# Kernel tuning notes

Hardware: AMD Instinct MI355X
Metric: run time of the kernel (lower is better)

The kernel has to match this reference:

```python
import jax, jax.numpy as jnp
import numpy as np

S = 1            # support_num
NEIGHBOR = 32    # neighbor_num for ball query
EPS = 1e-12

def _gather(t, idx):
    # t: (bs, N, C), idx: (bs, M, n) -> (bs, M, n, C)
    return jax.vmap(lambda tb, ib: tb[ib])(t, idx)

def _pick(t, idx):
    # t: (bs, M, C), idx: (bs, V) -> (bs, V, C)
    return jax.vmap(lambda tb, ib: tb[ib])(t, idx)

def _normalize(x, axis):
    return x / jnp.maximum(jnp.linalg.norm(x, axis=axis, keepdims=True), EPS)

def query_ball_point(radius, nsample, xyz, new_xyz):
    # PointNet++-style ball query: indices of first nsample points within radius,
    # missing slots filled with the first valid neighbor (self, since dist=0).
    sq = jnp.sum((new_xyz[:, :, None, :] - xyz[:, None, :, :]) ** 2, axis=-1)  # (bs,S,N)
    N = xyz.shape[1]
    idx = jnp.broadcast_to(jnp.arange(N), sq.shape)
    idx = jnp.where(sq > radius * radius, N, idx)
    idx = jnp.sort(idx, axis=-1)[:, :, :nsample]
    return jnp.where(idx == N, idx[:, :, :1], idx)

def _dir_norm(vertices, nbr_idx):
    nbrs = _gather(vertices, nbr_idx)                       # (bs,v,n,3)
    return _normalize(nbrs - vertices[:, :, None, :], axis=-1)

def conv_surface(nbr_idx, vertices, directions, K=32):
    # directions: (3, S*K)
    dn = _dir_norm(vertices, nbr_idx)
    theta = jax.nn.relu(jnp.einsum('bvnd,dk->bvnk', dn, _normalize(directions, 0)))
    bs, v, n, _ = theta.shape
    return theta.reshape(bs, v, n, S, K).max(axis=2).sum(axis=2)  # (bs,v,K)

def conv_layer(nbr_idx, vertices, fm, w, b, d, K=32):
    # w: (Cin,(S+1)*K), b: ((S+1)*K,), d: (3,S*K)
    dn = _dir_norm(vertices, nbr_idx)
    theta = jax.nn.relu(jnp.einsum('bvnd,dk->bvnk', dn, _normalize(d, 0)))  # (bs,v,n,S*K)
    f = jnp.einsum('bvc,ck->bvk', fm, w) + b                # (bs,v,(S+1)*K)
    center, support = f[..., :K], f[..., K:]
    sup = _gather(support, nbr_idx)                          # (bs,v,n,S*K)
    bs, v, n, _ = sup.shape
    act = (theta * sup).reshape(bs, v, n, S, K).max(axis=2).sum(axis=2)
    return center + act

def pool_layer(vertices, fm, radius, key, rate=4, nn_num=4):
    idx = query_ball_point(radius, nn_num, vertices, vertices)
    pooled = _gather(fm, idx).max(axis=2)                    # neighborhood max-pool
    v = vertices.shape[1]
    perm = jax.random.permutation(key, v)[: v // rate]       # random subsample (fixed key)
    return vertices[:, perm], pooled[:, perm]

def get_nearest_index(target, source):
    sq = jnp.sum((target[:, :, None, :] - source[:, None, :, :]) ** 2, axis=-1)
    return jnp.argmin(sq, axis=-1)                           # (bs, V_target)

def _forward(vertices, onehot, d0, w1, b1, dd1, w2, b2, dd2, w3, b3, dd3,
             w4, b4, dd4, w5, b5, dd5, w6, b6, dd6, w7, b7, dd7,
             cw1, cb1, cw2, cb2, cw3, cb3):
    relu = jax.nn.relu
    bs, V, _ = vertices.shape
    ni = query_ball_point(0.25, NEIGHBOR, vertices, vertices)
    fm0 = relu(conv_surface(ni, vertices, d0))
    fm1 = jnp.concatenate([fm0, relu(conv_layer(ni, vertices, fm0, w1, b1, dd1))], -1)
    fm2 = jnp.concatenate([fm1, relu(conv_layer(ni, vertices, fm1, w2, b2, dd2))], -1)
    v1, fp1 = pool_layer(vertices, fm2, 0.25, jax.random.fold_in(jax.random.key(42), 1))
    ni = query_ball_point(0.39, NEIGHBOR, v1, v1)
    fm3 = jnp.concatenate([fp1, relu(conv_layer(ni, v1, fp1, w3, b3, dd3))], -1)
    fm4 = jnp.concatenate([fm3, relu(conv_layer(ni, v1, fm3, w4, b4, dd4))], -1)
    fm5 = jnp.concatenate([fm4, relu(conv_layer(ni, v1, fm4, w5, b5, dd5))], -1)
    v2, fp2 = pool_layer(v1, fm5, 0.39, jax.random.fold_in(jax.random.key(42), 2))
    ni = query_ball_point(0.63, NEIGHBOR, v2, v2)
    fm6 = jnp.concatenate([fp2, relu(conv_layer(ni, v2, fp2, w6, b6, dd6))], -1)
    fm7 = jnp.concatenate([fm6, relu(conv_layer(ni, v2, fm6, w7, b7, dd7))], -1)
    f_global = fm7.max(axis=1)                               # (bs, 256)
    n1 = get_nearest_index(vertices, v1)
    n2 = get_nearest_index(vertices, v2)
    fuse = jnp.concatenate([
        fm0, fm1, fm2,
        _pick(fm3, n1), _pick(fm4, n1), _pick(fm5, n1),
        _pick(fm6, n2), _pick(fm7, n2),
        jnp.broadcast_to(f_global[:, None, :], (bs, V, f_global.shape[-1])),
        jnp.broadcast_to(onehot[:, None, :], (bs, V, onehot.shape[-1])),
    ], axis=-1)                                              # (bs, V, 1424)
    h = relu(jnp.einsum('bvc,oc->bvo', fuse, cw1) + cb1)
    h = relu(jnp.einsum('bvc,oc->bvo', h, cw2) + cb2)
    return jnp.einsum('bvc,oc->bvo', h, cw3) + cb3           # (bs, V, class_num)


def setup_inputs() -> dict:
    key = jax.random.key(0)
    ks = iter(jax.random.split(key, 40))
    bs, N, cat = 8, 2048, 16
    vertices = jax.random.uniform(next(ks), (bs, N, 3), dtype=jnp.float32)
    labels = jax.random.randint(next(ks), (bs,), 0, cat)
    onehot = jax.nn.one_hot(labels, cat, dtype=jnp.float32)
    def p(shape):
        return jax.random.normal(next(ks), shape, dtype=jnp.float32) * 0.05
    inp = {"vertices": vertices, "onehot": onehot, "d0": p((3, S * 32))}
    ins = [32, 64, 96, 128, 160, 192, 224]
    for i, c in enumerate(ins, start=1):
        inp[f"w{i}"] = p((c, (S + 1) * 32))
        inp[f"b{i}"] = p(((S + 1) * 32,))
        inp[f"dd{i}"] = p((3, S * 32))
    inp["cw1"] = p((1024, 1424)); inp["cb1"] = p((1024,))
    inp["cw2"] = p((512, 1024)); inp["cb2"] = p((512,))
    inp["cw3"] = p((50, 512)); inp["cb3"] = p((50,))
    return inp


def reference(vertices, onehot, d0, w1, b1, dd1, w2, b2, dd2, w3, b3, dd3,
              w4, b4, dd4, w5, b5, dd5, w6, b6, dd6, w7, b7, dd7,
              cw1, cb1, cw2, cb2, cw3, cb3):
    return _forward(vertices, onehot, d0, w1, b1, dd1, w2, b2, dd2, w3, b3, dd3,
                    w4, b4, dd4, w5, b5, dd5, w6, b6, dd6, w7, b7, dd7,
                    cw1, cb1, cw2, cb2, cw3, cb3)
```

## Files before the change

kernel.cpp:

```cpp
#include <hip/hip_runtime.h>
#include <hip/hip_bf16.h>

#define BS 8
#define V0 2048
#define V1N 512
#define V2N 128

typedef unsigned short ushort_t;
typedef __attribute__((ext_vector_type(8))) short bf16x8;
typedef __attribute__((ext_vector_type(4))) float f32x4;

__device__ __forceinline__ void tf2x32(unsigned k0, unsigned k1,
                                       unsigned x0, unsigned x1,
                                       unsigned &o0, unsigned &o1) {
  unsigned ks2 = k0 ^ k1 ^ 0x1BD11BDAu;
  x0 += k0; x1 += k1;
#define RR(r) { x0 += x1; x1 = (x1 << (r)) | (x1 >> (32 - (r))); x1 ^= x0; }
  RR(13) RR(15) RR(26) RR(6)   x0 += k1;  x1 += ks2 + 1u;
  RR(17) RR(29) RR(16) RR(24)  x0 += ks2; x1 += k0 + 2u;
  RR(13) RR(15) RR(26) RR(6)   x0 += k0;  x1 += k1 + 3u;
  RR(17) RR(29) RR(16) RR(24)  x0 += k1;  x1 += ks2 + 4u;
  RR(13) RR(15) RR(26) RR(6)   x0 += ks2; x1 += k0 + 5u;
#undef RR
  o0 = x0; o1 = x1;
}

__device__ __forceinline__ ushort_t f2bf(float f) {
  unsigned u = __float_as_uint(f);
  u += 0x7FFFu + ((u >> 16) & 1u);
  return (ushort_t)(u >> 16);
}

__device__ __forceinline__ float sqdist_f32(float cx, float cy, float cz,
                                            const float* p) {
  float dx = __fsub_rn(cx, p[0]);
  float dy = __fsub_rn(cy, p[1]);
  float dz = __fsub_rn(cz, p[2]);
  return __fadd_rn(__fadd_rn(__fmul_rn(dx, dx), __fmul_rn(dy, dy)),
                   __fmul_rn(dz, dz));
}

#define KP1 1472

#define PREP_BLKS 1025
#define QBP1_BLKS 512
__global__ __launch_bounds__(256) void misc1_kernel(
    int* __restrict__ rank, const float* __restrict__ cw1,
    const float* __restrict__ cw2, const float* __restrict__ cw3,
    const float* __restrict__ cb3, ushort_t* __restrict__ cw1b,
    ushort_t* __restrict__ cw2b, ushort_t* __restrict__ cw3b,
    float* __restrict__ cb3p, const float* __restrict__ pts,
    int* __restrict__ ni1) {
  int bid = blockIdx.x, tid = threadIdx.x;
  if (bid < 18) {
    __shared__ unsigned sb[2048];
    int seg, segfirst, n, base;
    if (bid < 8)       { seg = 0; segfirst = 0;  n = 2048; base = 0; }
    else if (bid < 16) { seg = 1; segfirst = 8;  n = 2048; base = 2048; }
    else               { seg = 2; segfirst = 16; n = 512;  base = 4096; }
    unsigned k0, k1, nk0, nk1, sk0, sk1;
    if (seg == 0) {
      tf2x32(0u, 42u, 0u, 1u, k0, k1);
      tf2x32(k0, k1, 0u, 1u, sk0, sk1);
    } else if (seg == 1) {
      tf2x32(0u, 42u, 0u, 1u, k0, k1);
      tf2x32(k0, k1, 0u, 0u, nk0, nk1);
      tf2x32(nk0, nk1, 0u, 1u, sk0, sk1);
    } else {
      tf2x32(0u, 42u, 0u, 2u, k0, k1);
      tf2x32(k0, k1, 0u, 1u, sk0, sk1);
    }
    for (int i = tid; i < n; i += 256) {
      unsigned o0, o1;
      tf2x32(sk0, sk1, 0u, (unsigned)i, o0, o1);
      sb[i] = o0 ^ o1;
    }
    __syncthreads();
    int tt = (bid - segfirst) * 256 + tid;
    unsigned bt = sb[tt];
    int cnt = 0;
#pragma unroll 8
    for (int s = 0; s < n; ++s) {
      unsigned bs = sb[s];
      cnt += (bs < bt) || (bs == bt && s < tt);
    }
    rank[base + tt] = cnt;
  } else if (bid < 18 + PREP_BLKS) {
    int c = (bid - 18) * 256 + tid;
    const int C1 = 1024 * (KP1 / 8);
    const int C2 = (512 * 1024) / 8;
    const int C3 = (128 * 512) / 8;
    if (c < C1) {
      int n = c / (KP1 / 8);
      int cc = c - n * (KP1 / 8);
      int k = cc * 8;
      bf16x8 o = (bf16x8){0, 0, 0, 0, 0, 0, 0, 0};
      if (k < 1424) {
        const float* src = cw1 + (size_t)n * 1424 + k;
        float4 lo = *(const float4*)src;
        float4 hi = *(const float4*)(src + 4);
        o[0] = (short)f2bf(lo.x); o[1] = (short)f2bf(lo.y);
        o[2] = (short)f2bf(lo.z); o[3] = (short)f2bf(lo.w);
        o[4] = (short)f2bf(hi.x); o[5] = (short)f2bf(hi.y);
        o[6] = (short)f2bf(hi.z); o[7] = (short)f2bf(hi.w);
      }
      *(bf16x8*)(cw1b + (size_t)c * 8) = o;
    } else if (c < C1 + C2) {
      int u = (c - C1) * 8;
      const float* src = cw2 + u;
      float4 lo = *(const float4*)src;
      float4 hi = *(const float4*)(src + 4);
      bf16x8 o;
      o[0] = (short)f2bf(lo.x); o[1] = (short)f2bf(lo.y);
      o[2] = (short)f2bf(lo.z); o[3] = (short)f2bf(lo.w);
      o[4] = (short)f2bf(hi.x); o[5] = (short)f2bf(hi.y);
      o[6] = (short)f2bf(hi.z); o[7] = (short)f2bf(hi.w);
      *(bf16x8*)(cw2b + u) = o;
    } else if (c < C1 + C2 + C3) {
      int u = (c - C1 - C2) * 8;
      int n = u >> 9, k = u & 511;
      bf16x8 o = (bf16x8){0, 0, 0, 0, 0, 0, 0, 0};
      if (n < 50) {
        const float* src = cw3 + (size_t)n * 512 + k;
        float4 lo = *(const float4*)src;
        float4 hi = *(const float4*)(src + 4);
        o[0] = (short)f2bf(lo.x); o[1] = (short)f2bf(lo.y);
        o[2] = (short)f2bf(lo.z); o[3] = (short)f2bf(lo.w);
        o[4] = (short)f2bf(hi.x); o[5] = (short)f2bf(hi.y);
        o[6] = (short)f2bf(hi.z); o[7] = (short)f2bf(hi.w);
      }
      *(bf16x8*)(cw3b + u) = o;
    } else if (c < C1 + C2 + C3 + 16) {
      int u = (c - C1 - C2 - C3) * 8;
#pragma unroll
      for (int e = 0; e < 8; ++e)
        cb3p[u + e] = (u + e) < 50 ? cb3[u + e] : 0.f;
    }
  } else {
    __shared__ float spts[V0 * 3];
    int bq = bid - 18 - PREP_BLKS;
    int qbase = bq * 32;
    int b = qbase >> 11;
    const float* base = pts + (size_t)b * V0 * 3;
    for (int i = tid; i < V0 * 3 / 4; i += 256)
      ((float4*)spts)[i] = ((const float4*)base)[i];
    __syncthreads();
    int lane = tid & 63, wv = tid >> 6;
    for (int rep = 0; rep < 8; ++rep) {
      int qoff = wv * 8 + rep;
      int qi = (qbase & 2047) + qoff;
      int wid = qbase + qoff;
      float cx = spts[qi * 3], cy = spts[qi * 3 + 1], cz = spts[qi * 3 + 2];
      int cnt = 0, idx0 = 0;
      for (int j0 = 0; j0 < V0; j0 += 64) {
        int j = j0 + lane;
        float d2 = sqdist_f32(cx, cy, cz, spts + (size_t)j * 3);
        bool in = (d2 <= 0.0625f);
        unsigned long long mask = __ballot(in);
        if (cnt == 0 && mask) idx0 = j0 + __builtin_ctzll(mask);
        if (in) {
          int rk = cnt + __popcll(mask & ((1ull << lane) - 1ull));
          if (rk < 32) ni1[(size_t)wid * 32 + rk] = j;
        }
        cnt += __popcll(mask);
        if (cnt >= 32) break;
      }
      for (int s = cnt + lane; s < 32; s += 64) ni1[(size_t)wid * 32 + s] = idx0;
    }
  }
}

__device__ __forceinline__ void dirn(const float* base, int v, int nb,
                                     float& ox, float& oy, float& oz) {
  float dx = __fsub_rn(base[nb * 3 + 0], base[v * 3 + 0]);
  float dy = __fsub_rn(base[nb * 3 + 1], base[v * 3 + 1]);
  float dz = __fsub_rn(base[nb * 3 + 2], base[v * 3 + 2]);
  float s2 = __fadd_rn(__fadd_rn(__fmul_rn(dx, dx), __fmul_rn(dy, dy)),
                       __fmul_rn(dz, dz));
  float nrm = fmaxf(__fsqrt_rn(s2), 1e-12f);
  ox = __fdiv_rn(dx, nrm); oy = __fdiv_rn(dy, nrm); oz = __fdiv_rn(dz, nrm);
}

__device__ __forceinline__ void norm_col(const float* d, int k,
                                         float& ox, float& oy, float& oz) {
  float x = d[k], y = d[32 + k], z = d[64 + k];
  float s2 = __fadd_rn(__fadd_rn(__fmul_rn(x, x), __fmul_rn(y, y)),
                       __fmul_rn(z, z));
  float nrm = fmaxf(__fsqrt_rn(s2), 1e-12f);
  ox = __fdiv_rn(x, nrm); oy = __fdiv_rn(y, nrm); oz = __fdiv_rn(z, nrm);
}

__global__ __launch_bounds__(256) void misc2_kernel(
    const int* __restrict__ rank, int* __restrict__ perm1,
    int* __restrict__ perm2, const float* __restrict__ pts,
    const int* __restrict__ ni, const float* __restrict__ d0,
    const float* __restrict__ w1, const float* __restrict__ b1,
    float* __restrict__ out, float* __restrict__ fn) {
  int bid = blockIdx.x, tid = threadIdx.x;
  if (bid == 0) {
    __shared__ int a1[2048];
    __shared__ int a2[2048];
    for (int i = tid; i < 2048; i += 256) a1[rank[i]] = i;
    __syncthreads();
    for (int i = tid; i < 2048; i += 256) a2[rank[2048 + i]] = a1[i];
    __syncthreads();
    for (int i = tid; i < 512; i += 256) perm1[i] = a2[i];
    for (int i = tid; i < 512; i += 256) a1[rank[4096 + i]] = i;
    __syncthreads();
    for (int i = tid; i < 128; i += 256) perm2[i] = a1[i];
    return;
  }
  __shared__ float sdir[3][32];
  __shared__ float sdn[8][32][3];
  __shared__ float sfm[8][32];
  if (tid < 32) {
    float x, y, z; norm_col(d0, tid, x, y, z);
    sdir[0][tid] = x; sdir[1][tid] = y; sdir[2][tid] = z;
  }
  int vloc = tid >> 5, k = tid & 31;
  size_t bvg = (size_t)(bid - 1) * 8 + vloc;
  int b = (int)(bvg >> 11), v = (int)(bvg & 2047);
  const float* base = pts + (size_t)b * V0 * 3;
  int nb = ni[bvg * 32 + k];
  float x, y, z; dirn(base, v, nb, x, y, z);
  sdn[vloc][k][0] = x; sdn[vloc][k][1] = y; sdn[vloc][k][2] = z;
  __syncthreads();
  float m = 0.f;
  for (int n = 0; n < 32; ++n) {
    float d = sdn[vloc][n][0] * sdir[0][k] + sdn[vloc][n][1] * sdir[1][k] +
              sdn[vloc][n][2] * sdir[2][k];
    m = fmaxf(m, fmaxf(d, 0.f));
  }
  out[bvg * 96 + k] = m;
  sfm[vloc][k] = m;
  __syncthreads();
  float a1v = b1[k], a2v = b1[k + 32];
  for (int c = 0; c < 32; ++c) {
    float vv = sfm[vloc][c];
    a1v += vv * w1[c * 64 + k];
    a2v += vv * w1[c * 64 + k + 32];
  }
  fn[bvg * 64 + k] = a1v;
  fn[bvg * 64 + k + 32] = a2v;
}

__global__ __launch_bounds__(256) void conv_act_kernel(
    const float* __restrict__ pts, const float* __restrict__ dd,
    const int* __restrict__ ni, const float* __restrict__ f,
    float* __restrict__ out, int Nv, int ldout, int colofs,
    const float* __restrict__ wn, const float* __restrict__ bn,
    float* __restrict__ fn) {
  __shared__ float sdir[3][32];
  __shared__ float sdn[8][32][3];
  __shared__ int sidx[8][32];
  __shared__ float sfm[8][256];
  int tid = threadIdx.x;
  if (tid < 32) {
    float x, y, z; norm_col(dd, tid, x, y, z);
    sdir[0][tid] = x; sdir[1][tid] = y; sdir[2][tid] = z;
  }
  int vloc = tid >> 5, k = tid & 31;
  size_t bvg = (size_t)blockIdx.x * 8 + vloc;
  int b = (int)(bvg / Nv), v = (int)(bvg % Nv);
  const float* base = pts + (size_t)b * Nv * 3;
  int nb = ni[bvg * 32 + k];
  float x, y, z; dirn(base, v, nb, x, y, z);
  sdn[vloc][k][0] = x; sdn[vloc][k][1] = y; sdn[vloc][k][2] = z;
  sidx[vloc][k] = nb;
  __syncthreads();
  float m = -INFINITY;
  size_t fb = (size_t)b * Nv * 64;
  for (int n = 0; n < 32; ++n) {
    float th = fmaxf(sdn[vloc][n][0] * sdir[0][k] + sdn[vloc][n][1] * sdir[1][k] +
                     sdn[vloc][n][2] * sdir[2][k], 0.f);
    float sup = f[fb + (size_t)sidx[vloc][n] * 64 + 32 + k];
    m = fmaxf(m, th * sup);
  }
  float center = f[bvg * 64 + k];
  float res = fmaxf(center + m, 0.f);
  out[bvg * ldout + colofs + k] = res;
  if (wn) {
    size_t rowbase = (size_t)blockIdx.x * 8;
#pragma unroll 1
    for (int r = 0; r < 8; ++r)
      if (tid < colofs) sfm[r][tid] = out[(rowbase + r) * ldout + tid];
    sfm[vloc][colofs + k] = res;
    __syncthreads();
    int cin = colofs + 32;
    float a1v = bn[k], a2v = bn[k + 32];
    for (int c = 0; c < cin; ++c) {
      float vv = sfm[vloc][c];
      a1v += vv * wn[c * 64 + k];
      a2v += vv * wn[c * 64 + k + 32];
    }
    fn[bvg * 64 + k] = a1v;
    fn[bvg * 64 + k + 32] = a2v;
  }
}

__global__ __launch_bounds__(256) void conv_act_qbp_kernel(
    const float* __restrict__ pts, int Nv, float rrq,
    const float* __restrict__ dd, int* __restrict__ ni_out,
    const float* __restrict__ f, float* __restrict__ out, int ldout,
    int colofs, const float* __restrict__ wn, const float* __restrict__ bn,
    float* __restrict__ fn) {
  __shared__ float spts[512 * 3];
  __shared__ float sdir[3][32];
  __shared__ float sdn[8][32][3];
  __shared__ int sni[8][32];
  __shared__ float sfm[8][256];
  int tid = threadIdx.x;
  int b = (blockIdx.x * 8) / Nv;
  int vbase = (blockIdx.x * 8) % Nv;
  const float* gp = pts + (size_t)b * Nv * 3;
  for (int i = tid; i < Nv * 3; i += 256) spts[i] = gp[i];
  if (tid < 32) {
    float x, y, z; norm_col(dd, tid, x, y, z);
    sdir[0][tid] = x; sdir[1][tid] = y; sdir[2][tid] = z;
  }
  __syncthreads();
  int lane = tid & 63, wv = tid >> 6;
  for (int rep = 0; rep < 2; ++rep) {
    int vl = wv * 2 + rep;
    int v = vbase + vl;
    float cx = spts[v * 3], cy = spts[v * 3 + 1], cz = spts[v * 3 + 2];
    int cnt = 0, idx0 = 0;
    for (int j0 = 0; j0 < Nv; j0 += 64) {
      int j = j0 + lane;
      float d2 = sqdist_f32(cx, cy, cz, spts + (size_t)j * 3);
      bool in = (d2 <= rrq);
      unsigned long long mask = __ballot(in);
      if (cnt == 0 && mask) idx0 = j0 + __builtin_ctzll(mask);
      if (in) {
        int rk = cnt + __popcll(mask & ((1ull << lane) - 1ull));
        if (rk < 32) sni[vl][rk] = j;
      }
      cnt += __popcll(mask);
      if (cnt >= 32) break;
    }
    for (int s = cnt + lane; s < 32; s += 64) sni[vl][s] = idx0;
  }
  __syncthreads();
  ni_out[(size_t)(blockIdx.x * 8) * 32 + tid] = sni[tid >> 5][tid & 31];
  int vloc = tid >> 5, k = tid & 31;
  size_t bvg = (size_t)blockIdx.x * 8 + vloc;
  int v = vbase + vloc;
  int nb = sni[vloc][k];
  float x, y, z; dirn(spts, v, nb, x, y, z);
  sdn[vloc][k][0] = x; sdn[vloc][k][1] = y; sdn[vloc][k][2] = z;
  __syncthreads();
  float m = -INFINITY;
  size_t fb = (size_t)b * Nv * 64;
  for (int n = 0; n < 32; ++n) {
    float th = fmaxf(sdn[vloc][n][0] * sdir[0][k] + sdn[vloc][n][1] * sdir[1][k] +
                     sdn[vloc][n][2] * sdir[2][k], 0.f);
    float sup = f[fb + (size_t)sni[vloc][n] * 64 + 32 + k];
    m = fmaxf(m, th * sup);
  }
  float center = f[bvg * 64 + k];
  float res = fmaxf(center + m, 0.f);
  out[bvg * ldout + colofs + k] = res;
  size_t rowbase = (size_t)blockIdx.x * 8;
#pragma unroll 1
  for (int r = 0; r < 8; ++r)
    if (tid < colofs) sfm[r][tid] = out[(rowbase + r) * ldout + tid];
  sfm[vloc][colofs + k] = res;
  __syncthreads();
  int cin = colofs + 32;
  float a1v = bn[k], a2v = bn[k + 32];
  for (int c = 0; c < cin; ++c) {
    float vv = sfm[vloc][c];
    a1v += vv * wn[c * 64 + k];
    a2v += vv * wn[c * 64 + k + 32];
  }
  fn[bvg * 64 + k] = a1v;
  fn[bvg * 64 + k + 32] = a2v;
}

__global__ __launch_bounds__(256) void pool_kernel(
    const float* __restrict__ pts_in, const float* __restrict__ fm_in,
    int ld_in, int C, int Nv_in, const int* __restrict__ perm, int Nv_out,
    float rr, float* __restrict__ pts_out, float* __restrict__ fm_out,
    int ld_out, const float* __restrict__ wn, const float* __restrict__ bn,
    float* __restrict__ fn) {
  __shared__ float spf[4][192];
  int wv = threadIdx.x >> 6;
  int lane = threadIdx.x & 63;
  int wid = blockIdx.x * 4 + wv;
  int b = wid / Nv_out, pp = wid - b * Nv_out;
  int v = perm[pp];
  const float* base = pts_in + (size_t)b * Nv_in * 3;
  float cx = base[v * 3], cy = base[v * 3 + 1], cz = base[v * 3 + 2];
  int nb[4]; int cnt = 0;
  for (int j0 = 0; j0 < Nv_in && cnt < 4; j0 += 64) {
    int j = j0 + lane;
    float d2 = sqdist_f32(cx, cy, cz, base + (size_t)j * 3);
    unsigned long long mask = __ballot(d2 <= rr);
    while (mask && cnt < 4) {
      int bp = __builtin_ctzll(mask);
      mask &= mask - 1;
      nb[cnt++] = j0 + bp;
    }
  }
  for (int q = cnt; q < 4; ++q) nb[q] = nb[0];
  if (lane < 3) pts_out[(size_t)wid * 3 + lane] = base[v * 3 + lane];
  size_t inrow = (size_t)b * Nv_in;
  size_t outrow = (size_t)wid * ld_out;
  for (int c = lane; c < C; c += 64) {
    float m = fm_in[(inrow + nb[0]) * ld_in + c];
    m = fmaxf(m, fm_in[(inrow + nb[1]) * ld_in + c]);
    m = fmaxf(m, fm_in[(inrow + nb[2]) * ld_in + c]);
    m = fmaxf(m, fm_in[(inrow + nb[3]) * ld_in + c]);
    fm_out[outrow + c] = m;
    spf[wv][c] = m;
  }
  __syncthreads();
  int o = threadIdx.x & 63, w_ = threadIdx.x >> 6;
  int wid0 = blockIdx.x * 4 + w_;
  float a = bn[o];
  for (int c = 0; c < C; ++c) a += spf[w_][c] * wn[c * 64 + o];
  fn[(size_t)wid0 * 64 + o] = a;
}

__global__ __launch_bounds__(256) void gmax_kernel(
    const float* __restrict__ fm, float* __restrict__ out) {
  __shared__ float red[8][32];
  int b = blockIdx.x >> 3, cg = blockIdx.x & 7;
  int vsub = threadIdx.x >> 5, cl = threadIdx.x & 31;
  int c = cg * 32 + cl;
  float m = -INFINITY;
  for (int v = vsub; v < V2N; v += 8)
    m = fmaxf(m, fm[((size_t)b * V2N + v) * 256 + c]);
  red[vsub][cl] = m;
  __syncthreads();
  if (vsub == 0) {
#pragma unroll
    for (int r = 1; r < 8; ++r) m = fmaxf(m, red[r][cl]);
    out[b * 256 + c] = m;
  }
}

__global__ __launch_bounds__(256) void fuse_row_kernel(
    const float* __restrict__ fm2, const float* __restrict__ fm5,
    const float* __restrict__ fm7, const float* __restrict__ fglob,
    const float* __restrict__ onehot, const float* __restrict__ verts,
    const float* __restrict__ v1, const float* __restrict__ v2,
    ushort_t* __restrict__ fuse_b) {
  __shared__ unsigned long long sred[8];
  __shared__ int sn12[2];
  int bv = blockIdx.x;
  int b = bv >> 11;
  int tid = threadIdx.x;
  int lane = tid & 63, wv = tid >> 6;
  float cx = verts[(size_t)bv * 3 + 0];
  float cy = verts[(size_t)bv * 3 + 1];
  float cz = verts[(size_t)bv * 3 + 2];
  unsigned long long b1 = ~0ull, b2 = ~0ull;
  const float* s1 = v1 + (size_t)b * V1N * 3;
  for (int j = tid; j < V1N; j += 256) {
    float d2 = sqdist_f32(cx, cy, cz, s1 + (size_t)j * 3);
    unsigned long long key =
        (((unsigned long long)__float_as_uint(d2)) << 32) | (unsigned)j;
    b1 = b1 < key ? b1 : key;
  }
  const float* s2 = v2 + (size_t)b * V2N * 3;
  if (tid < V2N) {
    float d2 = sqdist_f32(cx, cy, cz, s2 + (size_t)tid * 3);
    b2 = (((unsigned long long)__float_as_uint(d2)) << 32) | (unsigned)tid;
  }
#pragma unroll
  for (int off = 32; off > 0; off >>= 1) {
    unsigned long long o1 = __shfl_down(b1, off);
    unsigned long long o2 = __shfl_down(b2, off);
    b1 = b1 < o1 ? b1 : o1;
    b2 = b2 < o2 ? b2 : o2;
  }
  if (lane == 0) { sred[wv] = b1; sred[4 + wv] = b2; }
  __syncthreads();
  if (tid == 0) {
    unsigned long long m1 = sred[0], m2 = sred[4];
#pragma unroll
    for (int r = 1; r < 4; ++r) {
      m1 = m1 < sred[r] ? m1 : sred[r];
      m2 = m2 < sred[4 + r] ? m2 : sred[4 + r];
    }
    sn12[0] = (int)(m1 & 0xffffffffu);
    sn12[1] = (int)(m2 & 0xffffffffu);
  }
  __syncthreads();
  int sn1 = sn12[0], sn2 = sn12[1];
  const float* r2 = fm2 + (size_t)bv * 96;
  const float* r5 = fm5 + ((size_t)b * V1N + sn1) * 192;
  const float* r7 = fm7 + ((size_t)b * V2N + sn2) * 256;
  const float* rg = fglob + b * 256;
  const float* roh = onehot + b * 16;
  if (tid < KP1 / 8) {
    int c = tid * 8;
    const float* src = nullptr;
    if (c < 192) {
      int cc = (c < 32) ? c : (c < 96 ? c - 32 : c - 96);
      src = r2 + cc;
    } else if (c < 672) {
      int cc = (c < 320) ? c - 192 : (c < 480 ? c - 320 : c - 480);
      src = r5 + cc;
    } else if (c < 1152) {
      int cc = (c < 896) ? c - 672 : c - 896;
      src = r7 + cc;
    } else if (c < 1408) {
      src = rg + (c - 1152);
    } else if (c < 1424) {
      src = roh + (c - 1408);
    }
    float4 lo = make_float4(0.f, 0.f, 0.f, 0.f), hi = lo;
    if (src) { lo = *(const float4*)src; hi = *(const float4*)(src + 4); }
    bf16x8 o;
    o[0] = (short)f2bf(lo.x); o[1] = (short)f2bf(lo.y);
    o[2] = (short)f2bf(lo.z); o[3] = (short)f2bf(lo.w);
    o[4] = (short)f2bf(hi.x); o[5] = (short)f2bf(hi.y);
    o[6] = (short)f2bf(hi.z); o[7] = (short)f2bf(hi.w);
    *(bf16x8*)(fuse_b + (size_t)bv * KP1 + c) = o;
  }
}

typedef const __attribute__((address_space(1))) unsigned int gas_u32;
typedef __attribute__((address_space(3))) unsigned int las_u32;

__global__ __launch_bounds__(256) void gemm_mfma_nt(
    const ushort_t* __restrict__ A, const ushort_t* __restrict__ B,
    const float* __restrict__ bias, ushort_t* __restrict__ Cb,
    float* __restrict__ Cf, int K, int ldc, int nvalid, int mode) {
  __shared__ ushort_t As[128 * 64];
  __shared__ ushort_t Bs[128 * 64];
  int tid = threadIdx.x;
  int lane = tid & 63, w = tid >> 6;
  int wm = (w >> 1) * 64, wn = (w & 1) * 64;
  int nb = gridDim.x;
  int flat = blockIdx.x + nb * blockIdx.y;
  int xcd = flat & 7, slot = flat >> 3;
  int nidx = slot % nb;
  int mband = xcd + 8 * (slot / nb);
  int bm = mband * 128, bn = nidx * 128;
  f32x4 acc[4][4];
#pragma unroll
  for (int i = 0; i < 4; ++i)
#pragma unroll
    for (int j = 0; j < 4; ++j) acc[i][j] = (f32x4){0.f, 0.f, 0.f, 0.f};

  const ushort_t* gA[4];
  const ushort_t* gB[4];
  ushort_t* lA[4];
  ushort_t* lB[4];
  int rsub = lane >> 3;
  int scol = ((lane & 7) ^ rsub) * 8;
#pragma unroll
  for (int g = 0; g < 4; ++g) {
    int r = w * 32 + g * 8 + rsub;
    gA[g] = A + (size_t)(bm + r) * K + scol;
    gB[g] = B + (size_t)(bn + r) * K + scol;
    lA[g] = As + (w * 32 + g * 8) * 64;
    lB[g] = Bs + (w * 32 + g * 8) * 64;
  }
  int rA = lane & 15, q = lane >> 4;
  int r7 = rA & 7;

  for (int k0 = 0; k0 < K; k0 += 64) {
#pragma unroll
    for (int g = 0; g < 4; ++g)
      __builtin_amdgcn_global_load_lds((gas_u32*)(gA[g] + k0), (las_u32*)lA[g],
                                       16, 0, 0);
#pragma unroll
    for (int g = 0; g < 4; ++g)
      __builtin_amdgcn_global_load_lds((gas_u32*)(gB[g] + k0), (las_u32*)lB[g],
                                       16, 0, 0);
    __syncthreads();
#pragma unroll
    for (int s = 0; s < 2; ++s) {
      int pc = ((s * 4 + q) ^ r7) * 8;
      bf16x8 af[4], bfr[4];
#pragma unroll
      for (int i = 0; i < 4; ++i)
        af[i] = *(const bf16x8*)(As + (wm + i * 16 + rA) * 64 + pc);
#pragma unroll
      for (int j = 0; j < 4; ++j)
        bfr[j] = *(const bf16x8*)(Bs + (wn + j * 16 + rA) * 64 + pc);
#pragma unroll
      for (int i = 0; i < 4; ++i)
#pragma unroll
        for (int j = 0; j < 4; ++j)
          acc[i][j] = __builtin_amdgcn_mfma_f32_16x16x32_bf16(af[i], bfr[j],
                                                              acc[i][j], 0, 0, 0);
    }
    __syncthreads();
  }

  int rowq = (lane >> 4) * 4;
  int coll = lane & 15;
#pragma unroll
  for (int i = 0; i < 4; ++i) {
#pragma unroll
    for (int j = 0; j < 4; ++j) {
      int col = bn + wn + j * 16 + coll;
      float bi = bias[col];
#pragma unroll
      for (int r = 0; r < 4; ++r) {
        int row = bm + wm + i * 16 + rowq + r;
        float v = acc[i][j][r] + bi;
        if (mode == 0) {
          Cb[(size_t)row * ldc + col] = f2bf(fmaxf(v, 0.f));
        } else if (col < nvalid) {
          Cf[(size_t)row * ldc + col] = v;
        }
      }
    }
  }
}

__global__ __launch_bounds__(512, 2) void gemm256_mfma_nt(
    const ushort_t* __restrict__ A, const ushort_t* __restrict__ B,
    const float* __restrict__ bias, ushort_t* __restrict__ Cb,
    int K, int ldc) {
  __shared__ ushort_t As[2 * 256 * 64];
  __shared__ ushort_t Bs[2 * 256 * 64];
  int tid = threadIdx.x;
  int lane = tid & 63, w = tid >> 6;
  int wm = (w >> 2) * 128, wn = (w & 3) * 64;

  int flat = blockIdx.x;
  int xcd = flat & 7, slot = flat >> 3;
  int nidx = slot & 3, mband = xcd + 8 * (slot >> 2);
  int bm = mband * 256, bn = nidx * 256;

  f32x4 acc[8][4];
#pragma unroll
  for (int i = 0; i < 8; ++i)
#pragma unroll
    for (int j = 0; j < 4; ++j) acc[i][j] = (f32x4){0.f, 0.f, 0.f, 0.f};

  int rloc = tid >> 3, cch = tid & 7;
  int gc = (cch ^ (rloc & 7)) * 8;
  const ushort_t* gA[4];
  const ushort_t* gB[4];
#pragma unroll
  for (int i = 0; i < 4; ++i) {
    gA[i] = A + (size_t)(bm + i * 64 + rloc) * K + gc;
    gB[i] = B + (size_t)(bn + i * 64 + rloc) * K + gc;
  }
  int lofs = tid * 8;

  int rA = lane & 15, r7 = lane & 7;
  int qlane = lane >> 4;
  int pc0 = (qlane ^ r7) * 8;
  int pc1 = ((4 + qlane) ^ r7) * 8;

  int NT = K >> 6;

#pragma unroll
  for (int i = 0; i < 4; ++i) {
    __builtin_amdgcn_global_load_lds((gas_u32*)gA[i],
                                     (las_u32*)(As + i * 4096 + lofs), 16, 0, 0);
    gA[i] += 64;
  }
#pragma unroll
  for (int i = 0; i < 4; ++i) {
    __builtin_amdgcn_global_load_lds((gas_u32*)gB[i],
                                     (las_u32*)(Bs + i * 4096 + lofs), 16, 0, 0);
    gB[i] += 64;
  }

  for (int t = 0; t < NT; ++t) {
    int doff = (t & 1) * 16384;
    int poff = doff ^ 16384;

    asm volatile("s_waitcnt vmcnt(0)" ::: "memory");
    __builtin_amdgcn_sched_barrier(0);
    __builtin_amdgcn_s_barrier();
    __builtin_amdgcn_sched_barrier(0);

    if (t + 1 < NT) {
#pragma unroll
      for (int i = 0; i < 4; ++i) {
        __builtin_amdgcn_global_load_lds(
            (gas_u32*)gA[i], (las_u32*)(As + poff + i * 4096 + lofs), 16, 0, 0);
        gA[i] += 64;
      }
#pragma unroll
      for (int i = 0; i < 4; ++i) {
        __builtin_amdgcn_global_load_lds(
            (gas_u32*)gB[i], (las_u32*)(Bs + poff + i * 4096 + lofs), 16, 0, 0);
        gB[i] += 64;
      }
    }

    const ushort_t* Ab = As + doff;
    const ushort_t* Bb = Bs + doff;

    bf16x8 bfr0[4], bfr1[4];
#pragma unroll
    for (int fj = 0; fj < 4; ++fj)
      bfr0[fj] = *(const bf16x8*)(Bb + (wn + fj * 16 + rA) * 64 + pc0);
#pragma unroll
    for (int fj = 0; fj < 4; ++fj)
      bfr1[fj] = *(const bf16x8*)(Bb + (wn + fj * 16 + rA) * 64 + pc1);

    bf16x8 a0[4], a1[4];
#pragma unroll
    for (int fi = 0; fi < 4; ++fi)
      a0[fi] = *(const bf16x8*)(Ab + (wm + fi * 16 + rA) * 64 + pc0);

#pragma unroll
    for (int fi = 0; fi < 4; ++fi)
      a1[fi] = *(const bf16x8*)(Ab + (wm + fi * 16 + rA) * 64 + pc1);
#pragma unroll
    for (int fi = 0; fi < 4; ++fi)
#pragma unroll
      for (int fj = 0; fj < 4; ++fj)
        acc[fi][fj] = __builtin_amdgcn_mfma_f32_16x16x32_bf16(
            a0[fi], bfr0[fj], acc[fi][fj], 0, 0, 0);

#pragma unroll
    for (int fi = 0; fi < 4; ++fi)
      a0[fi] = *(const bf16x8*)(Ab + (wm + 64 + fi * 16 + rA) * 64 + pc0);
#pragma unroll
    for (int fi = 0; fi < 4; ++fi)
#pragma unroll
      for (int fj = 0; fj < 4; ++fj)
        acc[fi][fj] = __builtin_amdgcn_mfma_f32_16x16x32_bf16(
            a1[fi], bfr1[fj], acc[fi][fj], 0, 0, 0);

#pragma unroll
    for (int fi = 0; fi < 4; ++fi)
      a1[fi] = *(const bf16x8*)(Ab + (wm + 64 + fi * 16 + rA) * 64 + pc1);
#pragma unroll
    for (int fi = 0; fi < 4; ++fi)
#pragma unroll
      for (int fj = 0; fj < 4; ++fj)
        acc[4 + fi][fj] = __builtin_amdgcn_mfma_f32_16x16x32_bf16(
            a0[fi], bfr0[fj], acc[4 + fi][fj], 0, 0, 0);

#pragma unroll
    for (int fi = 0; fi < 4; ++fi)
#pragma unroll
      for (int fj = 0; fj < 4; ++fj)
        acc[4 + fi][fj] = __builtin_amdgcn_mfma_f32_16x16x32_bf16(
            a1[fi], bfr1[fj], acc[4 + fi][fj], 0, 0, 0);

    asm volatile("s_waitcnt lgkmcnt(0)" ::: "memory");
    __builtin_amdgcn_sched_barrier(0);
  }

  int rowq = (lane >> 4) * 4;
  int coll = lane & 15;
  float bi[4];
#pragma unroll
  for (int j = 0; j < 4; ++j) bi[j] = bias[bn + wn + j * 16 + coll];
#pragma unroll
  for (int i = 0; i < 8; ++i) {
#pragma unroll
    for (int j = 0; j < 4; ++j) {
      int col = bn + wn + j * 16 + coll;
#pragma unroll
      for (int r = 0; r < 4; ++r) {
        int row = bm + wm + i * 16 + rowq + r;
        float v = acc[i][j][r] + bi[j];
        Cb[(size_t)row * ldc + col] = f2bf(fmaxf(v, 0.f));
      }
    }
  }
}

extern "C" void kernel_launch(void* const* d_in, const int* in_sizes, int n_in,
                              void* d_out, int out_size, void* d_ws,
                              size_t ws_size, hipStream_t stream) {
  const float* vertices = (const float*)d_in[0];
  const float* onehot = (const float*)d_in[1];
  const float* d0 = (const float*)d_in[2];
  const float *w[8], *bb[8], *dd[8];
  for (int i = 1; i <= 7; ++i) {
    w[i] = (const float*)d_in[3 * i];
    bb[i] = (const float*)d_in[3 * i + 1];
    dd[i] = (const float*)d_in[3 * i + 2];
  }
  const float* cw1 = (const float*)d_in[24];
  const float* cb1 = (const float*)d_in[25];
  const float* cw2 = (const float*)d_in[26];
  const float* cb2 = (const float*)d_in[27];
  const float* cw3 = (const float*)d_in[28];
  const float* cb3 = (const float*)d_in[29];
  float* out = (float*)d_out;

  char* wsp = (char*)d_ws;
  size_t off = 0;
  auto alloc = [&](size_t bytes) -> void* {
    void* p = wsp + off;
    off += (bytes + 255) & ~(size_t)255;
    return p;
  };
  const int M = BS * V0;
  int* rank = (int*)alloc(4608 * 4);
  int* perm1 = (int*)alloc(512 * 4);
  int* perm2 = (int*)alloc(128 * 4);
  int* ni1 = (int*)alloc((size_t)BS * V0 * 32 * 4);
  int* ni2 = (int*)alloc((size_t)BS * V1N * 32 * 4);
  int* ni3 = (int*)alloc((size_t)BS * V2N * 32 * 4);
  float* fm2buf = (float*)alloc((size_t)BS * V0 * 96 * 4);
  float* fm5buf = (float*)alloc((size_t)BS * V1N * 192 * 4);
  float* fm7buf = (float*)alloc((size_t)BS * V2N * 256 * 4);
  float* fbuf = (float*)alloc((size_t)BS * V0 * 64 * 4);
  float* v1 = (float*)alloc((size_t)BS * V1N * 3 * 4);
  float* v2 = (float*)alloc((size_t)BS * V2N * 3 * 4);
  float* fglob = (float*)alloc((size_t)BS * 256 * 4);
  ushort_t* fuse_b = (ushort_t*)alloc((size_t)M * KP1 * 2);
  ushort_t* h1b = (ushort_t*)alloc((size_t)M * 1024 * 2);
  ushort_t* h2b = (ushort_t*)alloc((size_t)M * 512 * 2);
  ushort_t* cw1b = (ushort_t*)alloc((size_t)1024 * KP1 * 2);
  ushort_t* cw2b = (ushort_t*)alloc((size_t)512 * 1024 * 2);
  ushort_t* cw3b = (ushort_t*)alloc((size_t)128 * 512 * 2);
  float* cb3p = (float*)alloc(128 * 4);

  float rr1 = 0.0625f;
  float rr2 = (float)(0.39 * 0.39);
  float rr3 = (float)(0.63 * 0.63);

  misc1_kernel<<<18 + PREP_BLKS + QBP1_BLKS, 256, 0, stream>>>(
      rank, cw1, cw2, cw3, cb3, cw1b, cw2b, cw3b, cb3p, vertices, ni1);
  misc2_kernel<<<1 + BS * V0 / 8, 256, 0, stream>>>(
      rank, perm1, perm2, vertices, ni1, d0, w[1], bb[1], fm2buf, fbuf);
  conv_act_kernel<<<BS * V0 / 8, 256, 0, stream>>>(
      vertices, dd[1], ni1, fbuf, fm2buf, V0, 96, 32, w[2], bb[2], fbuf);
  conv_act_kernel<<<BS * V0 / 8, 256, 0, stream>>>(
      vertices, dd[2], ni1, fbuf, fm2buf, V0, 96, 64, nullptr, nullptr, nullptr);
  pool_kernel<<<BS * V1N / 4, 256, 0, stream>>>(
      vertices, fm2buf, 96, 96, V0, perm1, V1N, rr1, v1, fm5buf, 192,
      w[3], bb[3], fbuf);
  conv_act_qbp_kernel<<<BS * V1N / 8, 256, 0, stream>>>(
      v1, V1N, rr2, dd[3], ni2, fbuf, fm5buf, 192, 96, w[4], bb[4], fbuf);
  conv_act_kernel<<<BS * V1N / 8, 256, 0, stream>>>(
      v1, dd[4], ni2, fbuf, fm5buf, V1N, 192, 128, w[5], bb[5], fbuf);
  conv_act_kernel<<<BS * V1N / 8, 256, 0, stream>>>(
      v1, dd[5], ni2, fbuf, fm5buf, V1N, 192, 160, nullptr, nullptr, nullptr);
  pool_kernel<<<BS * V2N / 4, 256, 0, stream>>>(
      v1, fm5buf, 192, 192, V1N, perm2, V2N, rr2, v2, fm7buf, 256,
      w[6], bb[6], fbuf);
  conv_act_qbp_kernel<<<BS * V2N / 8, 256, 0, stream>>>(
      v2, V2N, rr3, dd[6], ni3, fbuf, fm7buf, 256, 192, w[7], bb[7], fbuf);
  conv_act_kernel<<<BS * V2N / 8, 256, 0, stream>>>(
      v2, dd[7], ni3, fbuf, fm7buf, V2N, 256, 224, nullptr, nullptr, nullptr);
  gmax_kernel<<<64, 256, 0, stream>>>(fm7buf, fglob);
  fuse_row_kernel<<<M, 256, 0, stream>>>(fm2buf, fm5buf, fm7buf, fglob, onehot,
                                         vertices, v1, v2, fuse_b);
  gemm256_mfma_nt<<<(M / 256) * (1024 / 256), 512, 0, stream>>>(
      fuse_b, cw1b, cb1, h1b, KP1, 1024);
  gemm_mfma_nt<<<dim3(512 / 128, M / 128), 256, 0, stream>>>(
      h1b, cw2b, cb2, h2b, nullptr, 1024, 512, 512, 0);
  gemm_mfma_nt<<<dim3(1, M / 128), 256, 0, stream>>>(
      h2b, cw3b, cb3p, nullptr, out, 512, 50, 50, 1);
}
```

Baseline: 394.0 us.

## Interleave GEMM prefetch and LDS reads into four barrier-separated MFMA phases

```diff
diff --git a/kernel.cpp b/kernel.cpp
--- a/kernel.cpp
+++ b/kernel.cpp
@@ -670,82 +670,68 @@
   for (int t = 0; t < NT; ++t) {
     int doff = (t & 1) * 16384;
     int poff = doff ^ 16384;
+    const ushort_t* Ab = As + doff;
+    const ushort_t* Bb = Bs + doff;
+    bool pf = (t + 1 < NT);
 
     asm volatile("s_waitcnt vmcnt(0)" ::: "memory");
     __builtin_amdgcn_sched_barrier(0);
     __builtin_amdgcn_s_barrier();
     __builtin_amdgcn_sched_barrier(0);
 
-    if (t + 1 < NT) {
-#pragma unroll
-      for (int i = 0; i < 4; ++i) {
-        __builtin_amdgcn_global_load_lds(
-            (gas_u32*)gA[i], (las_u32*)(As + poff + i * 4096 + lofs), 16, 0, 0);
-        gA[i] += 64;
+#pragma unroll
+    for (int q = 0; q < 4; ++q) {
+      int band = q >> 1, kh = q & 1;
+      int pck = kh ? pc1 : pc0;
+
+      bf16x8 af[4], bfq[4];
+#pragma unroll
+      for (int fi = 0; fi < 4; ++fi)
+        af[fi] = *(const bf16x8*)(Ab + (wm + band * 64 + fi * 16 + rA) * 64 + pck);
+#pragma unroll
+      for (int fj = 0; fj < 4; ++fj)
+        bfq[fj] = *(const bf16x8*)(Bb + (wn + fj * 16 + rA) * 64 + pck);
+
+      if (pf) {
+        if (q < 2) {
+          __builtin_amdgcn_global_load_lds(
+              (gas_u32*)gA[2 * q],
+              (las_u32*)(As + poff + (2 * q) * 4096 + lofs), 16, 0, 0);
+          __builtin_amdgcn_global_load_lds(
+              (gas_u32*)gA[2 * q + 1],
+              (las_u32*)(As + poff + (2 * q + 1) * 4096 + lofs), 16, 0, 0);
+          gA[2 * q] += 64;
+          gA[2 * q + 1] += 64;
+        } else {
+          int i = 2 * (q - 2);
+          __builtin_amdgcn_global_load_lds(
+              (gas_u32*)gB[i],
+              (las_u32*)(Bs + poff + i * 4096 + lofs), 16, 0, 0);
+          __builtin_amdgcn_global_load_lds(
+              (gas_u32*)gB[i + 1],
+              (las_u32*)(Bs + poff + (i + 1) * 4096 + lofs), 16, 0, 0);
+          gB[i] += 64;
+          gB[i + 1] += 64;
+        }
       }
-#pragma unroll
-      for (int i = 0; i < 4; ++i) {
-        __builtin_amdgcn_global_load_lds(
-            (gas_u32*)gB[i], (las_u32*)(Bs + poff + i * 4096 + lofs), 16, 0, 0);
-        gB[i] += 64;
-      }
-    }
-
-    const ushort_t* Ab = As + doff;
-    const ushort_t* Bb = Bs + doff;
-
-    bf16x8 bfr0[4], bfr1[4];
-#pragma unroll
-    for (int fj = 0; fj < 4; ++fj)
-      bfr0[fj] = *(const bf16x8*)(Bb + (wn + fj * 16 + rA) * 64 + pc0);
-#pragma unroll
-    for (int fj = 0; fj < 4; ++fj)
-      bfr1[fj] = *(const bf16x8*)(Bb + (wn + fj * 16 + rA) * 64 + pc1);
-
-    bf16x8 a0[4], a1[4];
-#pragma unroll
-    for (int fi = 0; fi < 4; ++fi)
-      a0[fi] = *(const bf16x8*)(Ab + (wm + fi * 16 + rA) * 64 + pc0);
-
-#pragma unroll
-    for (int fi = 0; fi < 4; ++fi)
-      a1[fi] = *(const bf16x8*)(Ab + (wm + fi * 16 + rA) * 64 + pc1);
-#pragma unroll
-    for (int fi = 0; fi < 4; ++fi)
-#pragma unroll
-      for (int fj = 0; fj < 4; ++fj)
-        acc[fi][fj] = __builtin_amdgcn_mfma_f32_16x16x32_bf16(
-            a0[fi], bfr0[fj], acc[fi][fj], 0, 0, 0);
-
-#pragma unroll
-    for (int fi = 0; fi < 4; ++fi)
-      a0[fi] = *(const bf16x8*)(Ab + (wm + 64 + fi * 16 + rA) * 64 + pc0);
-#pragma unroll
-    for (int fi = 0; fi < 4; ++fi)
-#pragma unroll
-      for (int fj = 0; fj < 4; ++fj)
-        acc[fi][fj] = __builtin_amdgcn_mfma_f32_16x16x32_bf16(
-            a1[fi], bfr1[fj], acc[fi][fj], 0, 0, 0);
-
-#pragma unroll
-    for (int fi = 0; fi < 4; ++fi)
-      a1[fi] = *(const bf16x8*)(Ab + (wm + 64 + fi * 16 + rA) * 64 + pc1);
-#pragma unroll
-    for (int fi = 0; fi < 4; ++fi)
-#pragma unroll
-      for (int fj = 0; fj < 4; ++fj)
-        acc[4 + fi][fj] = __builtin_amdgcn_mfma_f32_16x16x32_bf16(
-            a0[fi], bfr0[fj], acc[4 + fi][fj], 0, 0, 0);
-
-#pragma unroll
-    for (int fi = 0; fi < 4; ++fi)
-#pragma unroll
-      for (int fj = 0; fj < 4; ++fj)
-        acc[4 + fi][fj] = __builtin_amdgcn_mfma_f32_16x16x32_bf16(
-            a1[fi], bfr1[fj], acc[4 + fi][fj], 0, 0, 0);
-
-    asm volatile("s_waitcnt lgkmcnt(0)" ::: "memory");
-    __builtin_amdgcn_sched_barrier(0);
+
+      __builtin_amdgcn_sched_barrier(0);
+      __builtin_amdgcn_s_barrier();
+      asm volatile("s_waitcnt lgkmcnt(0)" ::: "memory");
+      __builtin_amdgcn_sched_barrier(0);
+
+      __builtin_amdgcn_s_setprio(1);
+#pragma unroll
+      for (int fi = 0; fi < 4; ++fi)
+#pragma unroll
+        for (int fj = 0; fj < 4; ++fj)
+          acc[band * 4 + fi][fj] = __builtin_amdgcn_mfma_f32_16x16x32_bf16(
+              af[fi], bfq[fj], acc[band * 4 + fi][fj], 0, 0, 0);
+      __builtin_amdgcn_s_setprio(0);
+      __builtin_amdgcn_sched_barrier(0);
+      __builtin_amdgcn_s_barrier();
+      __builtin_amdgcn_sched_barrier(0);
+    }
   }
 
   int rowq = (lane >> 4) * 4;
```

After: 387.5 us. About the same (-1.6%).
